# Optimization experiments

Measured on AMD Instinct MI355X. Metric: run time of the kernel, lower is better.

The kernel has to match this reference:

```python
import jax, jax.numpy as jnp
import numpy as np

B, M, D = 32768, 4096, 128


def setup_inputs() -> dict:
    key = jax.random.key(0)
    k1, k2 = jax.random.split(key)
    local_stats = jax.random.normal(k1, (B, D), dtype=jnp.float32)
    memory = jax.random.normal(k2, (M, D), dtype=jnp.float32)
    return {"local_stats": local_stats, "memory": memory}


def reference(local_stats, memory):
    # attention logits: [B, M] = x @ memory^T (unscaled single-head attention read)
    logits = jnp.einsum("bd,md->bm", local_stats, memory)
    attn = jax.nn.softmax(logits, axis=1)          # [B, M]
    global_stats = jnp.einsum("bm,md->bd", attn, memory)  # [B, D]
    return global_stats
```

## Files before the change

kernel.cpp:

```cpp
#include <hip/hip_runtime.h>
#include <hip/hip_bf16.h>
#include <stdint.h>


typedef float    f32x16 __attribute__((ext_vector_type(16)));
typedef _Float16 f16x8  __attribute__((ext_vector_type(8)));
typedef uint32_t u32;

#define AS1 __attribute__((address_space(1)))
#define AS3 __attribute__((address_space(3)))

#define D_DIM 128
#define B_ROWS 32768
#define TILE_HW 8192
#define HALF_TILES 64

#if __has_builtin(__builtin_amdgcn_exp2f)
#define EXP2F(x) __builtin_amdgcn_exp2f(x)
#else
#define EXP2F(x) exp2f(x)
#endif

__device__ __forceinline__ uint16_t f32_to_f16_bits(float x) {
    _Float16 h = (_Float16)x;
    uint16_t r; __builtin_memcpy(&r, &h, 2);
    return r;
}

__global__ void prep_frags(const float* __restrict__ mem,
                           uint16_t* __restrict__ kv) {
    int t = blockIdx.x * blockDim.x + threadIdx.x;
    int lane = t & 63;
    int fi = t >> 6;
    int f8 = fi & 7, mt = fi >> 3;
    size_t base = (size_t)mt * TILE_HW;
    {
        int m  = mt * 32 + (lane & 31);
        int d0 = f8 * 16 + (lane >> 5) * 8;
        const float* src = mem + (size_t)m * D_DIM + d0;
        #pragma unroll
        for (int e = 0; e < 8; ++e)
            kv[base + f8 * 512 + lane * 8 + e] = f32_to_f16_bits(src[e]);
    }
    {
        int dt = fi & 3, ks = (fi >> 2) & 1;
        int d  = dt * 32 + (lane & 31);
        int m0 = mt * 32 + ks * 16 + (lane >> 5) * 8;
        #pragma unroll
        for (int e = 0; e < 8; ++e)
            kv[base + 4096 + f8 * 512 + lane * 8 + e] =
                f32_to_f16_bits(mem[(size_t)(m0 + e) * D_DIM + d]);
    }
}


#define STAGE(t_, wb_) do {                                                   \
    const char* g_ = (const char*)(kv + (size_t)(tilebase + (t_)) * TILE_HW); \
    char* l_ = (char*)&sbuf[wb_][0];                                          \
    _Pragma("unroll")                                                         \
    for (int j_ = 0; j_ < 4; ++j_) {                                          \
        int ch_ = wave * 4 + j_;                                              \
        __builtin_amdgcn_global_load_lds(                                     \
            (const AS1 char*)(g_ + ch_ * 1024 + lane * 16),                   \
            (AS3 char*)(l_ + ch_ * 1024), 16, 0, 0);                          \
    }                                                                         \
} while (0)

#define MFMA_F16(a_, b_, c_) __builtin_amdgcn_mfma_f32_32x32x16_f16(a_, b_, c_, 0, 0, 0)

#define QK(bp_, s_) do {                                                      \
    f16x8 kh_[8];                                                             \
    _Pragma("unroll")                                                         \
    for (int kk_ = 0; kk_ < 8; ++kk_)                                         \
        kh_[kk_] = *(const f16x8*)((bp_) + kk_ * 512);                        \
    f32x16 sA_, sB_;                                                          \
    _Pragma("unroll")                                                         \
    for (int i_ = 0; i_ < 16; ++i_) { sA_[i_] = 0.f; sB_[i_] = 0.f; }         \
    sA_ = MFMA_F16(kh_[0], qh[0], sA_);                                       \
    sB_ = MFMA_F16(kh_[1], qh[1], sB_);                                       \
    sA_ = MFMA_F16(kh_[2], qh[2], sA_);                                       \
    sB_ = MFMA_F16(kh_[3], qh[3], sB_);                                       \
    sA_ = MFMA_F16(kh_[4], qh[4], sA_);                                       \
    sB_ = MFMA_F16(kh_[5], qh[5], sB_);                                       \
    sA_ = MFMA_F16(kh_[6], qh[6], sA_);                                       \
    sB_ = MFMA_F16(kh_[7], qh[7], sB_);                                       \
    s_ = sA_ + sB_;                                                           \
} while (0)

#define SMX_PV(s_, bp_) do {                                                  \
    float a0=fmaxf(s_[0],s_[1]),  a1=fmaxf(s_[2],s_[3]);                      \
    float a2=fmaxf(s_[4],s_[5]),  a3=fmaxf(s_[6],s_[7]);                      \
    float a4=fmaxf(s_[8],s_[9]),  a5=fmaxf(s_[10],s_[11]);                    \
    float a6=fmaxf(s_[12],s_[13]),a7=fmaxf(s_[14],s_[15]);                    \
    float tmax = fmaxf(fmaxf(fmaxf(a0,a1),fmaxf(a2,a3)),                      \
                       fmaxf(fmaxf(a4,a5),fmaxf(a6,a7)));                     \
    tmax = fmaxf(tmax, __shfl_xor(tmax, 32));                                 \
    if (__any(tmax > m_run + 8.0f)) {                    \
        float mn = fmaxf(m_run, tmax);                                        \
        float fr = EXP2F(m_run - mn);                                         \
        m_run = mn; l_run *= fr;                                              \
        _Pragma("unroll")                                                     \
        for (int r_ = 0; r_ < 16; ++r_) {                                     \
            O0[r_] *= fr; O1[r_] *= fr; O2[r_] *= fr; O3[r_] *= fr;           \
        }                                                                     \
    }                                                                         \
    _Pragma("unroll")                                                         \
    for (int r_ = 0; r_ < 16; ++r_) s_[r_] = EXP2F(s_[r_] - m_run);           \
    { float q0s=s_[0]+s_[1],  q1s=s_[2]+s_[3],  q2s=s_[4]+s_[5],  q3s=s_[6]+s_[7];   \
      float q4s=s_[8]+s_[9],  q5s=s_[10]+s_[11],q6s=s_[12]+s_[13],q7s=s_[14]+s_[15]; \
      l_run += ((q0s+q1s)+(q2s+q3s)) + ((q4s+q5s)+(q6s+q7s)); }               \
    u32 c_[8];                                                                \
    _Pragma("unroll")                                                         \
    for (int j_ = 0; j_ < 8; ++j_)                                            \
        asm("v_cvt_pkrtz_f16_f32 %0, %1, %2"                                  \
            : "=v"(c_[j_]) : "v"(s_[2*j_]), "v"(s_[2*j_+1]));                 \
    asm("v_permlane32_swap_b32 %0, %1" : "+v"(c_[0]), "+v"(c_[2]));           \
    asm("v_permlane32_swap_b32 %0, %1" : "+v"(c_[1]), "+v"(c_[3]));           \
    asm("v_permlane32_swap_b32 %0, %1" : "+v"(c_[4]), "+v"(c_[6]));           \
    asm("v_permlane32_swap_b32 %0, %1" : "+v"(c_[5]), "+v"(c_[7]));           \
    f16x8 pf0_, pf1_;                                                         \
    { u32 w_[4] = {c_[0], c_[1], c_[2], c_[3]}; __builtin_memcpy(&pf0_, w_, 16); } \
    { u32 w_[4] = {c_[4], c_[5], c_[6], c_[7]}; __builtin_memcpy(&pf1_, w_, 16); } \
    f16x8 vf_[8];                                                             \
    _Pragma("unroll")                                                         \
    for (int f_ = 0; f_ < 8; ++f_)                                            \
        vf_[f_] = *(const f16x8*)((bp_) + 4096 + f_ * 512);                   \
    O0 = MFMA_F16(vf_[0], pf0_, O0);                                          \
    O1 = MFMA_F16(vf_[1], pf0_, O1);                                          \
    O2 = MFMA_F16(vf_[2], pf0_, O2);                                          \
    O3 = MFMA_F16(vf_[3], pf0_, O3);                                          \
    O0 = MFMA_F16(vf_[4], pf1_, O0);                                          \
    O1 = MFMA_F16(vf_[5], pf1_, O1);                                          \
    O2 = MFMA_F16(vf_[6], pf1_, O2);                                          \
    O3 = MFMA_F16(vf_[7], pf1_, O3);                                          \
} while (0)

#define PSTORE_TILE(Ot_, t_) do {                                             \
    _Pragma("unroll")                                                         \
    for (int g_ = 0; g_ < 4; ++g_) {                                          \
        float4 v_ = { Ot_[4*g_+0], Ot_[4*g_+1], Ot_[4*g_+2], Ot_[4*g_+3] };   \
        int d_ = (t_) * 32 + 8 * g_ + 4 * hi32;                               \
        *(float4*)(prow + d_) = v_;                                           \
    }                                                                         \
} while (0)

__global__ __launch_bounds__(256, 2)
void attn_main(const float* __restrict__ qin,
               const uint16_t* __restrict__ kv,
               float* __restrict__ out0,
               float* __restrict__ pout1,
               float2* __restrict__ pml) {
    __shared__ uint16_t sbuf[4][TILE_HW];

    const int lane = threadIdx.x & 63;
    const int wave = threadIdx.x >> 6;
    const int half = blockIdx.x & 1;
    const int tilebase = half * HALF_TILES;
    const int q0   = (blockIdx.x >> 1) * 128 + wave * 32;
    const int qrow = q0 + (lane & 31);
    const int hi32 = lane >> 5;

    f16x8 qh[8];
    {
        const float LOG2E = 1.44269504088896340736f;
        #pragma unroll
        for (int kk = 0; kk < 8; ++kk) {
            const float* src = qin + (size_t)qrow * D_DIM + kk * 16 + hi32 * 8;
            float4 a = *(const float4*)(src);
            float4 b = *(const float4*)(src + 4);
            float xs[8] = {a.x, a.y, a.z, a.w, b.x, b.y, b.z, b.w};
            #pragma unroll
            for (int e = 0; e < 8; ++e)
                qh[kk][e] = (_Float16)(xs[e] * LOG2E);
        }
    }

    f32x16 O0, O1, O2, O3;
    #pragma unroll
    for (int i = 0; i < 16; ++i) { O0[i]=0.f; O1[i]=0.f; O2[i]=0.f; O3[i]=0.f; }
    float m_run = -1e30f, l_run = 0.f;

    STAGE(0, 0);
    STAGE(1, 1);
    __syncthreads();

    #pragma unroll 1
    for (int t = 0; t < HALF_TILES; t += 2) {
        if (t + 2 < HALF_TILES) STAGE(t + 2, (t + 2) & 3);
        if (t + 3 < HALF_TILES) STAGE(t + 3, (t + 3) & 3);
        const uint16_t* bp0 = &sbuf[t & 3][0] + lane * 8;
        const uint16_t* bp1 = &sbuf[(t + 1) & 3][0] + lane * 8;

        f32x16 s0, s1;
        QK(bp0, s0);
        QK(bp1, s1);
        SMX_PV(s0, bp0);
        SMX_PV(s1, bp1);
        __syncthreads();
    }

    l_run += __shfl_xor(l_run, 32);
    float* prow = (half == 0 ? out0 : pout1) + (size_t)qrow * D_DIM;
    PSTORE_TILE(O0, 0); PSTORE_TILE(O1, 1);
    PSTORE_TILE(O2, 2); PSTORE_TILE(O3, 3);
    if (lane < 32) {
        pml[(size_t)half * B_ROWS + qrow] = make_float2(m_run, l_run);
    }
}

__global__ __launch_bounds__(256)
void merge_halves(const float* __restrict__ pout1,
                  const float2* __restrict__ pml,
                  float* __restrict__ out) {
    int idx  = blockIdx.x * 256 + threadIdx.x;
    int row  = idx >> 5;
    int c4   = idx & 31;
    float2 a = pml[row];
    float2 b = pml[B_ROWS + row];
    float mn = fmaxf(a.x, b.x);
    float wa = EXP2F(a.x - mn);
    float wb = EXP2F(b.x - mn);
    float rinv = 1.0f / (a.y * wa + b.y * wb);
    float4* O = (float4*)(out + (size_t)row * D_DIM) + c4;
    const float4* P1 = (const float4*)(pout1 + (size_t)row * D_DIM) + c4;
    float4 p0 = *O, p1 = *P1;
    float4 v;
    v.x = (p0.x * wa + p1.x * wb) * rinv;
    v.y = (p0.y * wa + p1.y * wb) * rinv;
    v.z = (p0.z * wa + p1.z * wb) * rinv;
    v.w = (p0.w * wa + p1.w * wb) * rinv;
    *O = v;
}

extern "C" void kernel_launch(void* const* d_in, const int* in_sizes, int n_in,
                              void* d_out, int out_size, void* d_ws, size_t ws_size,
                              hipStream_t stream) {
    const float* local_stats = (const float*)d_in[0];
    const float* memory      = (const float*)d_in[1];
    float* out = (float*)d_out;

    uint16_t* kv   = (uint16_t*)d_ws;
    float*   pout1 = (float*)((char*)d_ws + 2 * 1024 * 1024);
    float2*  pml   = (float2*)((char*)pout1 + (size_t)B_ROWS * D_DIM * 4);

    prep_frags<<<256, 256, 0, stream>>>(memory, kv);
    attn_main<<<512, 256, 0, stream>>>(local_stats, kv, out, pout1, pml);
    merge_halves<<<4096, 256, 0, stream>>>(pout1, pml, out);
}
```

Measured before the change: 101.4 us.

## Split K/V fragment buffers; stage only K in LDS, load V directly from global

Splits the prepared fp16 memory fragments into separate K and V arrays. Only K tiles are now staged into shared memory via async global-to-LDS loads, while V fragments are loaded per wave straight from global memory into registers at the start of each iteration. This halves LDS footprint and LDS read traffic, but adds per-wave global/L2 traffic for V (each of 4 waves reloads the same V tile) and raises register pressure, with V load latency exposed unless overlapped by the QK/softmax work.

```diff
diff --git a/kernel.cpp b/kernel.cpp
--- a/kernel.cpp
+++ b/kernel.cpp
@@ -12,7 +12,7 @@
 
 #define D_DIM 128
 #define B_ROWS 32768
-#define TILE_HW 8192
+#define KTILE_HW 4096
 #define HALF_TILES 64
 
 #if __has_builtin(__builtin_amdgcn_exp2f)
@@ -28,19 +28,20 @@
 }
 
 __global__ void prep_frags(const float* __restrict__ mem,
-                           uint16_t* __restrict__ kv) {
+                           uint16_t* __restrict__ kws,
+                           uint16_t* __restrict__ vws) {
     int t = blockIdx.x * blockDim.x + threadIdx.x;
     int lane = t & 63;
     int fi = t >> 6;
     int f8 = fi & 7, mt = fi >> 3;
-    size_t base = (size_t)mt * TILE_HW;
+    size_t base = (size_t)mt * KTILE_HW;
     {
         int m  = mt * 32 + (lane & 31);
         int d0 = f8 * 16 + (lane >> 5) * 8;
         const float* src = mem + (size_t)m * D_DIM + d0;
         #pragma unroll
         for (int e = 0; e < 8; ++e)
-            kv[base + f8 * 512 + lane * 8 + e] = f32_to_f16_bits(src[e]);
+            kws[base + f8 * 512 + lane * 8 + e] = f32_to_f16_bits(src[e]);
     }
     {
         int dt = fi & 3, ks = (fi >> 2) & 1;
@@ -48,18 +49,18 @@
         int m0 = mt * 32 + ks * 16 + (lane >> 5) * 8;
         #pragma unroll
         for (int e = 0; e < 8; ++e)
-            kv[base + 4096 + f8 * 512 + lane * 8 + e] =
+            vws[base + f8 * 512 + lane * 8 + e] =
                 f32_to_f16_bits(mem[(size_t)(m0 + e) * D_DIM + d]);
     }
 }
 
 
-#define STAGE(t_, wb_) do {                                                   \
-    const char* g_ = (const char*)(kv + (size_t)(tilebase + (t_)) * TILE_HW); \
+#define STAGE_K(t_, wb_) do {                                                 \
+    const char* g_ = (const char*)(kws + (size_t)(tilebase + (t_)) * KTILE_HW);\
     char* l_ = (char*)&sbuf[wb_][0];                                          \
     _Pragma("unroll")                                                         \
-    for (int j_ = 0; j_ < 4; ++j_) {                                          \
-        int ch_ = wave * 4 + j_;                                              \
+    for (int j_ = 0; j_ < 2; ++j_) {                                          \
+        int ch_ = wave * 2 + j_;                                              \
         __builtin_amdgcn_global_load_lds(                                     \
             (const AS1 char*)(g_ + ch_ * 1024 + lane * 16),                   \
             (AS3 char*)(l_ + ch_ * 1024), 16, 0, 0);                          \
@@ -67,6 +68,13 @@
 } while (0)
 
 #define MFMA_F16(a_, b_, c_) __builtin_amdgcn_mfma_f32_32x32x16_f16(a_, b_, c_, 0, 0, 0)
+
+#define VLOAD(t_, vf_) do {                                                   \
+    const uint16_t* vg_ = vws + (size_t)(tilebase + (t_)) * KTILE_HW + lane * 8;\
+    _Pragma("unroll")                                                         \
+    for (int f_ = 0; f_ < 8; ++f_)                                            \
+        vf_[f_] = *(const f16x8*)(vg_ + f_ * 512);                            \
+} while (0)
 
 #define QK(bp_, s_) do {                                                      \
     f16x8 kh_[8];                                                             \
@@ -87,7 +95,7 @@
     s_ = sA_ + sB_;                                                           \
 } while (0)
 
-#define SMX_PV(s_, bp_) do {                                                  \
+#define SMX_PV(s_, vf_) do {                                                  \
     float a0=fmaxf(s_[0],s_[1]),  a1=fmaxf(s_[2],s_[3]);                      \
     float a2=fmaxf(s_[4],s_[5]),  a3=fmaxf(s_[6],s_[7]);                      \
     float a4=fmaxf(s_[8],s_[9]),  a5=fmaxf(s_[10],s_[11]);                    \
@@ -121,10 +129,6 @@
     f16x8 pf0_, pf1_;                                                         \
     { u32 w_[4] = {c_[0], c_[1], c_[2], c_[3]}; __builtin_memcpy(&pf0_, w_, 16); } \
     { u32 w_[4] = {c_[4], c_[5], c_[6], c_[7]}; __builtin_memcpy(&pf1_, w_, 16); } \
-    f16x8 vf_[8];                                                             \
-    _Pragma("unroll")                                                         \
-    for (int f_ = 0; f_ < 8; ++f_)                                            \
-        vf_[f_] = *(const f16x8*)((bp_) + 4096 + f_ * 512);                   \
     O0 = MFMA_F16(vf_[0], pf0_, O0);                                          \
     O1 = MFMA_F16(vf_[1], pf0_, O1);                                          \
     O2 = MFMA_F16(vf_[2], pf0_, O2);                                          \
@@ -146,11 +150,12 @@
 
 __global__ __launch_bounds__(256, 2)
 void attn_main(const float* __restrict__ qin,
-               const uint16_t* __restrict__ kv,
+               const uint16_t* __restrict__ kws,
+               const uint16_t* __restrict__ vws,
                float* __restrict__ out0,
                float* __restrict__ pout1,
                float2* __restrict__ pml) {
-    __shared__ uint16_t sbuf[4][TILE_HW];
+    __shared__ uint16_t sbuf[4][KTILE_HW];
 
     const int lane = threadIdx.x & 63;
     const int wave = threadIdx.x >> 6;
@@ -180,22 +185,26 @@
     for (int i = 0; i < 16; ++i) { O0[i]=0.f; O1[i]=0.f; O2[i]=0.f; O3[i]=0.f; }
     float m_run = -1e30f, l_run = 0.f;
 
-    STAGE(0, 0);
-    STAGE(1, 1);
+    STAGE_K(0, 0);
+    STAGE_K(1, 1);
     __syncthreads();
 
     #pragma unroll 1
     for (int t = 0; t < HALF_TILES; t += 2) {
-        if (t + 2 < HALF_TILES) STAGE(t + 2, (t + 2) & 3);
-        if (t + 3 < HALF_TILES) STAGE(t + 3, (t + 3) & 3);
+        if (t + 2 < HALF_TILES) STAGE_K(t + 2, (t + 2) & 3);
+        if (t + 3 < HALF_TILES) STAGE_K(t + 3, (t + 3) & 3);
         const uint16_t* bp0 = &sbuf[t & 3][0] + lane * 8;
         const uint16_t* bp1 = &sbuf[(t + 1) & 3][0] + lane * 8;
+
+        f16x8 vf0[8], vf1[8];
+        VLOAD(t, vf0);
+        VLOAD(t + 1, vf1);
 
         f32x16 s0, s1;
         QK(bp0, s0);
         QK(bp1, s1);
-        SMX_PV(s0, bp0);
-        SMX_PV(s1, bp1);
+        SMX_PV(s0, vf0);
+        SMX_PV(s1, vf1);
         __syncthreads();
     }
 
@@ -239,11 +248,12 @@
     const float* memory      = (const float*)d_in[1];
     float* out = (float*)d_out;
 
-    uint16_t* kv   = (uint16_t*)d_ws;
+    uint16_t* kws  = (uint16_t*)d_ws;
+    uint16_t* vws  = kws + 128 * KTILE_HW;
     float*   pout1 = (float*)((char*)d_ws + 2 * 1024 * 1024);
     float2*  pml   = (float2*)((char*)pout1 + (size_t)B_ROWS * D_DIM * 4);
 
-    prep_frags<<<256, 256, 0, stream>>>(memory, kv);
-    attn_main<<<512, 256, 0, stream>>>(local_stats, kv, out, pout1, pml);
+    prep_frags<<<256, 256, 0, stream>>>(memory, kws, vws);
+    attn_main<<<512, 256, 0, stream>>>(local_stats, kws, vws, out, pout1, pml);
     merge_halves<<<4096, 256, 0, stream>>>(pout1, pml, out);
 }
```

Result: no change. 102.7 us (+1.3%).
